# Optimization experiments

Hardware: AMD Instinct MI355X
Metric: run time of the kernel (lower is better)

The kernel has to match this reference:

```python
import jax, jax.numpy as jnp
import numpy as np
import math

# Model dims
B, S, D, H = 2, 2048, 1024, 16
DH = D // H  # 64
TAU = 0.2
EPS = 1e-5

# Unit-scaling scale factors (constraint = gmean of fwd/bwd scales)
# Linear: gmean(fan_in**-0.5, fan_out**-0.5) = (fan_in*fan_out)**-0.25
# Matmul (m,k)@(k,n): gmean(k**-0.5, n**-0.5, m**-0.5) = (m*k*n)**(-1/6)
# Softmax over dim n: gmean(n/1.31, n/1.65) (empirical constants from unit_scaling)
# GELU: gmean(1/0.588, 1/0.675)
MM_SCALE = (S * S * DH) ** (-1.0 / 6.0)
SM_SCALE = S / math.sqrt(1.31 * 1.65)
GELU_SCALE = (0.588 * 0.675) ** -0.5
SQRT_TAU = math.sqrt(TAU)
SQRT_1MTAU = math.sqrt(1.0 - TAU)


def u_linear(x, w, b=None):
    fan_out, fan_in = w.shape
    scale = (fan_in * fan_out) ** -0.25
    y = x @ w.T
    if b is not None:
        y = y + b
    return y * scale


def layer_norm(x, w, b):
    m = jnp.mean(x, axis=-1, keepdims=True)
    v = jnp.mean(jnp.square(x - m), axis=-1, keepdims=True)
    return (x - m) * jax.lax.rsqrt(v + EPS) * w + b


def setup_inputs() -> dict:
    key = jax.random.key(0)
    ks = jax.random.split(key, 8)
    return {
        "x": jax.random.normal(ks[0], (B, S, D), jnp.float32),
        "w_qkv": jax.random.normal(ks[1], (3 * D, D), jnp.float32),
        "w_o": jax.random.normal(ks[2], (D, D), jnp.float32),
        "w1": jax.random.normal(ks[3], (4 * D, D), jnp.float32),
        "b1": jnp.zeros((4 * D,), jnp.float32),
        "w2": jax.random.normal(ks[4], (D, 4 * D), jnp.float32),
        "b2": jnp.zeros((D,), jnp.float32),
        "ln1_w": jnp.ones((D,), jnp.float32),
        "ln1_b": jnp.zeros((D,), jnp.float32),
        "ln2_w": jnp.ones((D,), jnp.float32),
        "ln2_b": jnp.zeros((D,), jnp.float32),
    }


def reference(x, w_qkv, w_o, w1, b1, w2, b2, ln1_w, ln1_b, ln2_w, ln2_b):
    # --- MHSA branch (residual_split forward is identity; tau enters at add) ---
    skip = x
    h = layer_norm(x, ln1_w, ln1_b)
    qkv = u_linear(h, w_qkv)  # [B,S,3D]
    # einops 'b s (d z h) -> z b h s d' with z=3, h=H
    qkv = qkv.reshape(B, S, DH, 3, H)
    q = jnp.transpose(qkv[:, :, :, 0, :], (0, 3, 1, 2))  # [B,H,S,DH]
    k = jnp.transpose(qkv[:, :, :, 1, :], (0, 3, 1, 2))
    v = jnp.transpose(qkv[:, :, :, 2, :], (0, 3, 1, 2))
    scores = jnp.einsum("bhsd,bhtd->bhst", q, k) * MM_SCALE
    attn = jax.nn.softmax(scores, axis=-1) * SM_SCALE
    # dropout: eval mode -> identity
    av = jnp.einsum("bhst,bhtd->bhsd", attn, v) * MM_SCALE
    av = jnp.transpose(av, (0, 2, 1, 3)).reshape(B, S, D)  # b h s d -> b s (h d)
    attn_out = u_linear(av, w_o)
    x = SQRT_TAU * attn_out + SQRT_1MTAU * skip  # residual_add

    # --- MLP branch ---
    skip = x
    h = layer_norm(x, ln2_w, ln2_b)
    h = u_linear(h, w1, b1)
    h = jax.nn.gelu(h, approximate=False) * GELU_SCALE
    h = u_linear(h, w2, b2)
    return SQRT_TAU * h + SQRT_1MTAU * skip
```

## Files before the change

kernel.cpp:

```cpp
#include <hip/hip_runtime.h>
#include <hip/hip_bf16.h>
#include <math.h>

typedef __hip_bfloat16 bf16;
typedef __attribute__((ext_vector_type(8))) short short8;
typedef __attribute__((ext_vector_type(4))) float floatx4;

#define B_   2
#define S_   2048
#define D_   1024
#define H_   16
#define DH_  64
#define BS_  4096
#define D3_  3072
#define DF_  4096

__device__ __forceinline__ float tof(float v) { return v; }
__device__ __forceinline__ float tof(bf16 v) { return __bfloat162float(v); }

__device__ __forceinline__ void gload_lds16(const bf16* g, bf16* l) {
  __builtin_amdgcn_global_load_lds(
      (const __attribute__((address_space(1))) unsigned int*)g,
      (__attribute__((address_space(3))) unsigned int*)l, 16, 0, 0);
}

#define VMCNT(n) asm volatile("s_waitcnt vmcnt(" #n ")" ::: "memory")

__global__ __launch_bounds__(256) void cvt_f32_bf16(
    const float* __restrict__ in, bf16* __restrict__ out, int n4) {
  int i = blockIdx.x * 256 + threadIdx.x;
  if (i >= n4) return;
  float4 v = ((const float4*)in)[i];
  bf16 o[4] = {__float2bfloat16(v.x), __float2bfloat16(v.y),
               __float2bfloat16(v.z), __float2bfloat16(v.w)};
  ((ulong1*)out)[i] = *(ulong1*)o;
}

__global__ __launch_bounds__(256) void cvt_qkv_o(
    const float* __restrict__ wqkv, const float* __restrict__ wo,
    bf16* __restrict__ wqb, bf16* __restrict__ wob) {
  const int g = blockIdx.x * 256 + threadIdx.x;
  if (g < 786432) {
    const int n2 = g >> 8;
    const int col = (g & 255) * 4;
    const int z = n2 >> 10, hh = (n2 >> 6) & 15, d = n2 & 63;
    const int n = d * 48 + z * 16 + hh;
    float4 v = *(const float4*)(wqkv + (size_t)n * 1024 + col);
    bf16 o[4] = {__float2bfloat16(v.x), __float2bfloat16(v.y),
                 __float2bfloat16(v.z), __float2bfloat16(v.w)};
    *(unsigned long long*)(wqb + (size_t)n2 * 1024 + col) =
        *(unsigned long long*)o;
  } else {
    const int g2 = g - 786432;
    float4 v = ((const float4*)wo)[g2];
    bf16 o[4] = {__float2bfloat16(v.x), __float2bfloat16(v.y),
                 __float2bfloat16(v.z), __float2bfloat16(v.w)};
    ((unsigned long long*)wob)[g2] = *(unsigned long long*)o;
  }
}

template <bool FUSE, bool INIT, typename TA, typename TS>
__global__ __launch_bounds__(256) void resid_ln_kernel(
    const TA* __restrict__ a, const TA* __restrict__ a2,
    const TS* __restrict__ skip,
    const float* __restrict__ w, const float* __restrict__ bias,
    bf16* __restrict__ hout, float st, float s1t,
    float* __restrict__ oinit, const float* __restrict__ b2,
    float cb, float cs) {
  const int row = blockIdx.x;
  const int tid = threadIdx.x;
  const int base = tid * 4;
  const size_t roff = (size_t)row * D_;

  float xv[4];
#pragma unroll
  for (int i = 0; i < 4; i++) {
    float v = tof(a[roff + base + i]);
    if (FUSE) v = st * (v + tof(a2[roff + base + i]))
                  + s1t * tof(skip[roff + base + i]);
    xv[i] = v;
  }
  if (INIT) {
#pragma unroll
    for (int i = 0; i < 4; i++)
      oinit[roff + base + i] = cs * xv[i] + cb * b2[base + i];
  }

  float ls = 0.f, lq = 0.f;
#pragma unroll
  for (int i = 0; i < 4; i++) { ls += xv[i]; lq += xv[i] * xv[i]; }

  __shared__ float ssum[256];
  __shared__ float ssq[256];
  ssum[tid] = ls; ssq[tid] = lq;
  __syncthreads();
  for (int off = 128; off > 0; off >>= 1) {
    if (tid < off) { ssum[tid] += ssum[tid + off]; ssq[tid] += ssq[tid + off]; }
    __syncthreads();
  }
  const float mean = ssum[0] * (1.0f / D_);
  const float var  = ssq[0] * (1.0f / D_) - mean * mean;
  const float rstd = rsqrtf(var + 1e-5f);

#pragma unroll
  for (int i = 0; i < 4; i++) {
    float v = (xv[i] - mean) * rstd * w[base + i] + bias[base + i];
    hout[roff + base + i] = __float2bfloat16(v);
  }
}

__global__ __launch_bounds__(256) void reduce_ffn2(
    const bf16* __restrict__ p0, const bf16* __restrict__ p1,
    float* __restrict__ out, float sc) {
  const size_t i = ((size_t)blockIdx.x * 256 + threadIdx.x) * 8;
  short8 a = *(const short8*)(p0 + i);
  short8 b = *(const short8*)(p1 + i);
  bf16 t0[8], t1[8];
  *(short8*)t0 = a; *(short8*)t1 = b;
  float4 o0 = *(float4*)(out + i);
  float4 o1 = *(float4*)(out + i + 4);
#pragma unroll
  for (int e = 0; e < 4; e++) {
    ((float*)&o0)[e] += sc * (__bfloat162float(t0[e]) + __bfloat162float(t1[e]));
    ((float*)&o1)[e] += sc * (__bfloat162float(t0[e + 4]) + __bfloat162float(t1[e + 4]));
  }
  *(float4*)(out + i) = o0;
  *(float4*)(out + i + 4) = o1;
}

template <int EPI, int NSPLIT, typename TC>
__global__ __launch_bounds__(512, 2) void gemm_mfma256(
    const bf16* __restrict__ A, const bf16* __restrict__ Bw,
    TC* __restrict__ C, int M, int N, int K, float scale,
    const float* __restrict__ bias, float st) {
  __shared__ __align__(16) bf16 As[2][2][128][64];
  __shared__ __align__(16) bf16 Bs[2][2][128][64];

  const int tid = threadIdx.x;
  const int lane = tid & 63;
  const int w = tid >> 6;
  const int wm = w >> 2;
  const int wn = w & 3;
  const int quad = lane >> 4;
  const int l16 = lane & 15;

  const int nbx = N >> 8;
  const int nwg = nbx * (M >> 8) * NSPLIT;
  int bid = blockIdx.x;
  bid = (bid & 7) * (nwg >> 3) + (bid >> 3);
  const int split = bid & (NSPLIT - 1);
  const int tile = bid / NSPLIT;
  const size_t bm = (size_t)(tile / nbx) * 256;
  const size_t bn = (size_t)(tile % nbx) * 256;
  const int lda = K * NSPLIT;
  const int koff = split * K;

  const bf16* gsrc[4][2];
  bf16* ldsp[4][2];
#pragma unroll
  for (int i = 0; i < 2; i++) {
    const int G = tid + i * 512;
    const int cr = G >> 3;
    const int gs8 = ((G & 7) ^ (cr & 7)) * 8;
    const int ra = ((cr >> 6) << 7) + (cr & 63);
    const int rb = ((cr >> 5) << 6) + (cr & 31);
    gsrc[0][i] = A  + (bm + ra) * (size_t)lda + koff + gs8;
    gsrc[2][i] = A  + (bm + ra + 64) * (size_t)lda + koff + gs8;
    gsrc[1][i] = Bw + (bn + rb) * (size_t)lda + koff + gs8;
    gsrc[3][i] = Bw + (bn + rb + 32) * (size_t)lda + koff + gs8;
    ldsp[0][i] = &As[0][0][0][0] + G * 8;
    ldsp[2][i] = &As[0][1][0][0] + G * 8;
    ldsp[1][i] = &Bs[0][0][0][0] + G * 8;
    ldsp[3][i] = &Bs[0][1][0][0] + G * 8;
  }

  auto STAGE = [&](int c, int tn) {
    const int boff = (tn & 1) * 16384;
    gload_lds16(gsrc[c][0] + (size_t)tn * 64, ldsp[c][0] + boff);
    gload_lds16(gsrc[c][1] + (size_t)tn * 64, ldsp[c][1] + boff);
  };

  const int ksw0 = (quad ^ (l16 & 7)) * 8;
  const int ksw1 = ((4 + quad) ^ (l16 & 7)) * 8;

  floatx4 acc[8][4];
#pragma unroll
  for (int i = 0; i < 8; i++)
#pragma unroll
    for (int j = 0; j < 4; j++) acc[i][j] = {0.f, 0.f, 0.f, 0.f};

  short8 af[4][2], bv[2][2];

  auto READ_A = [&](int b, int h) {
#pragma unroll
    for (int mf = 0; mf < 4; mf++) {
      const bf16* p = &As[b][h][wm * 64 + mf * 16 + l16][0];
      af[mf][0] = *(const short8*)(p + ksw0);
      af[mf][1] = *(const short8*)(p + ksw1);
    }
  };
  auto READ_B = [&](int b, int bh) {
#pragma unroll
    for (int nf = 0; nf < 2; nf++) {
      const bf16* p = &Bs[b][bh][wn * 32 + nf * 16 + l16][0];
      bv[nf][0] = *(const short8*)(p + ksw0);
      bv[nf][1] = *(const short8*)(p + ksw1);
    }
  };
  auto MFMA16 = [&](int mb, int nb) {
#pragma unroll
    for (int mf = 0; mf < 4; mf++)
#pragma unroll
      for (int nf = 0; nf < 2; nf++) {
        floatx4 c = acc[mb + mf][nb + nf];
        c = __builtin_amdgcn_mfma_f32_16x16x32_bf16(af[mf][0], bv[nf][0], c, 0, 0, 0);
        c = __builtin_amdgcn_mfma_f32_16x16x32_bf16(af[mf][1], bv[nf][1], c, 0, 0, 0);
        acc[mb + mf][nb + nf] = c;
      }
  };

  STAGE(0, 0); STAGE(1, 0); STAGE(2, 0); STAGE(3, 0);
  VMCNT(4);
  __builtin_amdgcn_s_barrier();
  __builtin_amdgcn_sched_barrier(0);

  const int NT = K >> 6;
#pragma unroll 1
  for (int t = 0; t < NT; t++) {
    const int b = t & 1;
    const bool nl = (t + 1 < NT);
    READ_A(b, 0);
    READ_B(b, 0);
    if (nl) STAGE(0, t + 1);
    __builtin_amdgcn_s_barrier();
    __builtin_amdgcn_sched_barrier(0);
    __builtin_amdgcn_s_setprio(1);
    MFMA16(0, 0);
    __builtin_amdgcn_s_setprio(0);
    if (nl) { VMCNT(2); } else { VMCNT(0); }
    __builtin_amdgcn_s_barrier();
    __builtin_amdgcn_sched_barrier(0);
    READ_B(b, 1);
    if (nl) STAGE(1, t + 1);
    __builtin_amdgcn_s_barrier();
    __builtin_amdgcn_sched_barrier(0);
    __builtin_amdgcn_s_setprio(1);
    MFMA16(0, 2);
    __builtin_amdgcn_s_setprio(0);
    __builtin_amdgcn_s_barrier();
    __builtin_amdgcn_sched_barrier(0);
    READ_A(b, 1);
    if (nl) STAGE(2, t + 1);
    __builtin_amdgcn_s_barrier();
    __builtin_amdgcn_sched_barrier(0);
    __builtin_amdgcn_s_setprio(1);
    MFMA16(4, 2);
    __builtin_amdgcn_s_setprio(0);
    __builtin_amdgcn_s_barrier();
    __builtin_amdgcn_sched_barrier(0);
    READ_B(b, 0);
    if (nl) STAGE(3, t + 1);
    __builtin_amdgcn_s_barrier();
    __builtin_amdgcn_sched_barrier(0);
    __builtin_amdgcn_s_setprio(1);
    MFMA16(4, 0);
    __builtin_amdgcn_s_setprio(0);
    if (nl) { VMCNT(4); } else { VMCNT(0); }
    __builtin_amdgcn_s_barrier();
    __builtin_amdgcn_sched_barrier(0);
  }

  float sc_eff = scale;
  if (EPI == 2) sc_eff = (bn < 1024) ? st : scale;
  float bias4[4];
  if (EPI == 1) {
#pragma unroll
    for (int j = 0; j < 4; j++) bias4[j] = bias[bn + wn * 64 + j * 16 + l16];
  }
  const size_t poff = (size_t)split * M * N;
#pragma unroll
  for (int mi = 0; mi < 8; mi++) {
    const size_t r0 = bm + wm * 128 + (mi >> 2) * 64 + (mi & 3) * 16 + quad * 4;
#pragma unroll
    for (int r = 0; r < 4; r++) {
      const size_t rowoff = (r0 + r) * (size_t)N + bn + wn * 64 + l16;
#pragma unroll
      for (int j = 0; j < 4; j++) {
        float v = acc[mi][j][r];
        if (EPI == 0 || EPI == 2) {
          ((bf16*)C)[rowoff + j * 16] = __float2bfloat16(v * sc_eff);
        } else if (EPI == 1) {
          float u = (v + bias4[j]) * scale;
          float tt = u * (0.7978845608f + 0.0356774081f * u * u);
          float e = __builtin_amdgcn_exp2f(tt * 2.8853900818f);
          float th = 1.0f - 2.0f * __builtin_amdgcn_rcpf(e + 1.0f);
          ((bf16*)C)[rowoff + j * 16] =
              __float2bfloat16(0.5f * u * (1.0f + th) * st);
        } else if (EPI == 3) {
          ((float*)C)[poff + rowoff + j * 16] = v * scale;
        } else {
          ((bf16*)C)[poff + rowoff + j * 16] = __float2bfloat16(v);
        }
      }
    }
  }
}

__global__ __launch_bounds__(512) void flash_attn_mfma(
    const bf16* __restrict__ qkv, bf16* __restrict__ att, float out_scale) {
  const int qb = blockIdx.x * 128;
  const int h = blockIdx.y, b = blockIdx.z;
  const int tid = threadIdx.x;
  const int lane = tid & 63;
  const int wv = tid >> 6;
  const int quad = lane >> 4;
  const int l16 = lane & 15;

  __shared__ __align__(16) bf16 Ks[2][64][72];
  __shared__ __align__(16) bf16 Vt[2][64][72];
  __shared__ __align__(16) bf16 Ps[128][64];

  const bf16* Qb_ = qkv + (size_t)b * S_ * D3_ + h * DH_;
  const bf16* Kb_ = Qb_ + 1024;
  const bf16* Vb_ = Qb_ + 2048;

  short8 bq0, bq1;
  {
    const bf16* qrow = Qb_ + (size_t)(qb + wv * 16 + l16) * D3_ + quad * 8;
    bq0 = *(const short8*)(qrow);
    bq1 = *(const short8*)(qrow + 32);
  }

  float l_part = 0.f;
  floatx4 o[4];
#pragma unroll
  for (int fd = 0; fd < 4; fd++) o[fd] = {0.f, 0.f, 0.f, 0.f};

  const int prow = wv * 16 + l16;
  const int psw = (prow & 7) << 4;
  char* pbase = (char*)&Ps[0][0] + prow * 128;

  const int kr = tid >> 3, ko = (tid & 7) * 8;
  const int vj = tid & 63, vd = (tid >> 6) * 8;

  uint4 kreg = *(const uint4*)(Kb_ + (size_t)kr * D3_ + ko);
  uint4 vreg = *(const uint4*)(Vb_ + (size_t)vj * D3_ + vd);

  int cur = 0;
  for (int t = 0; t < S_ / 64; t++) {
    *(uint4*)&Ks[cur][kr][ko] = kreg;
    {
      bf16 tmp[8];
      *(uint4*)tmp = vreg;
#pragma unroll
      for (int e = 0; e < 8; e++) Vt[cur][vd + e][vj] = tmp[e];
    }
    __syncthreads();

    {
      const int tn = (t + 1 < S_ / 64) ? t + 1 : t;
      kreg = *(const uint4*)(Kb_ + (size_t)(tn * 64 + kr) * D3_ + ko);
      vreg = *(const uint4*)(Vb_ + (size_t)(tn * 64 + vj) * D3_ + vd);
    }

    float st[4][4];
    __builtin_amdgcn_s_setprio(1);
#pragma unroll
    for (int fk = 0; fk < 4; fk++) {
      short8 ak0 = *(const short8*)&Ks[cur][fk * 16 + l16][quad * 8];
      short8 ak1 = *(const short8*)&Ks[cur][fk * 16 + l16][32 + quad * 8];
      floatx4 acc = {0.f, 0.f, 0.f, 0.f};
      acc = __builtin_amdgcn_mfma_f32_16x16x32_bf16(ak0, bq0, acc, 0, 0, 0);
      acc = __builtin_amdgcn_mfma_f32_16x16x32_bf16(ak1, bq1, acc, 0, 0, 0);
#pragma unroll
      for (int r = 0; r < 4; r++) st[fk][r] = acc[r];
    }
    __builtin_amdgcn_s_setprio(0);

#pragma unroll
    for (int fk = 0; fk < 4; fk++) {
      bf16 pk[4];
#pragma unroll
      for (int r = 0; r < 4; r++) {
        const float p = exp2f(st[fk][r]);
        l_part += p;
        pk[r] = __float2bfloat16(p);
      }
      *(uint2*)(pbase + ((fk * 32 + quad * 8) ^ psw)) = *(uint2*)pk;
    }

    short8 ap0 = *(const short8*)(pbase + ((quad * 16) ^ psw));
    short8 ap1 = *(const short8*)(pbase + ((64 + quad * 16) ^ psw));
    __builtin_amdgcn_s_setprio(1);
#pragma unroll
    for (int fd = 0; fd < 4; fd++) {
      short8 bv0 = *(const short8*)&Vt[cur][fd * 16 + l16][quad * 8];
      short8 bv1 = *(const short8*)&Vt[cur][fd * 16 + l16][32 + quad * 8];
      o[fd] = __builtin_amdgcn_mfma_f32_16x16x32_bf16(ap0, bv0, o[fd], 0, 0, 0);
      o[fd] = __builtin_amdgcn_mfma_f32_16x16x32_bf16(ap1, bv1, o[fd], 0, 0, 0);
    }
    __builtin_amdgcn_s_setprio(0);

    cur ^= 1;
  }

  l_part += __shfl_xor(l_part, 16);
  l_part += __shfl_xor(l_part, 32);
#pragma unroll
  for (int r = 0; r < 4; r++) {
    const float lq = __shfl(l_part, quad * 4 + r, 64);
    const float sc = out_scale / lq;
    const size_t base =
        ((size_t)(b * S_ + qb + wv * 16 + quad * 4 + r)) * D_ + h * DH_;
#pragma unroll
    for (int fd = 0; fd < 4; fd++)
      att[base + fd * 16 + l16] = __float2bfloat16(o[fd][r] * sc);
  }
}

extern "C" void kernel_launch(void* const* d_in, const int* in_sizes, int n_in,
                              void* d_out, int out_size, void* d_ws, size_t ws_size,
                              hipStream_t stream) {
  const float* x     = (const float*)d_in[0];
  const float* w_qkv = (const float*)d_in[1];
  const float* w_o   = (const float*)d_in[2];
  const float* w1    = (const float*)d_in[3];
  const float* b1    = (const float*)d_in[4];
  const float* w2    = (const float*)d_in[5];
  const float* b2    = (const float*)d_in[6];
  const float* ln1w  = (const float*)d_in[7];
  const float* ln1b  = (const float*)d_in[8];
  const float* ln2w  = (const float*)d_in[9];
  const float* ln2b  = (const float*)d_in[10];
  float* out = (float*)d_out;
  bf16* ws  = (bf16*)d_ws;

  bf16* h1   = ws;
  bf16* wqb  = ws + 4194304;
  bf16* qkv  = ws + 8388608;
  bf16* att  = ws + 20971520;
  bf16* wob  = ws + 25165824;
  float* Po  = (float*)ws;
  bf16* w1b  = ws + 16777216;
  bf16* h2   = ws + 20971520;
  bf16* g    = ws;
  bf16* w2b  = ws + 16777216;
  bf16* Pf   = ws + 20971520;

  const float MM_SCALE   = (float)pow((double)S_ * S_ * DH_, -1.0 / 6.0);
  const float SM_SCALE   = (float)((double)S_ / sqrt(1.31 * 1.65));
  const float GELU_SCALE = (float)pow(0.588 * 0.675, -0.5);
  const float SQRT_TAU   = (float)sqrt(0.2);
  const float SQRT_1MT   = (float)sqrt(0.8);
  const float LOG2E      = 1.4426950408889634f;
  const float qkv_scale  = (float)pow((double)D_ * D3_, -0.25);
  const float o_scale    = (float)pow((double)D_ * D_, -0.25);
  const float w1_scale   = (float)pow((double)D_ * DF_, -0.25);
  const float w2_scale   = (float)pow((double)DF_ * D_, -0.25);

  cvt_qkv_o<<<4096, 256, 0, stream>>>(w_qkv, w_o, wqb, wob);
  resid_ln_kernel<false, false, float, float><<<BS_, 256, 0, stream>>>(
      x, nullptr, nullptr, ln1w, ln1b, h1, 0.f, 0.f, nullptr, nullptr, 0.f, 0.f);
  gemm_mfma256<2, 1, bf16><<<dim3(192), 512, 0, stream>>>(
      h1, wqb, qkv, BS_, D3_, D_, qkv_scale, nullptr,
      qkv_scale * MM_SCALE * LOG2E);
  flash_attn_mfma<<<dim3(S_ / 128, H_, B_), 512, 0, stream>>>(
      qkv, att, SM_SCALE * MM_SCALE);
  cvt_f32_bf16<<<(DF_ * D_ / 4 + 255) / 256, 256, 0, stream>>>(w1, w1b, DF_ * D_ / 4);
  gemm_mfma256<3, 2, float><<<dim3(128), 512, 0, stream>>>(
      att, wob, Po, BS_, D_, D_ / 2, o_scale, nullptr, 0.f);
  resid_ln_kernel<true, true, float, float><<<BS_, 256, 0, stream>>>(
      Po, Po + (size_t)BS_ * D_, x, ln2w, ln2b, h2, SQRT_TAU, SQRT_1MT,
      out, b2, SQRT_TAU * w2_scale, SQRT_1MT);
  gemm_mfma256<1, 1, bf16><<<dim3(256), 512, 0, stream>>>(
      h2, w1b, g, BS_, DF_, D_, w1_scale, b1, GELU_SCALE);
  cvt_f32_bf16<<<(D_ * DF_ / 4 + 255) / 256, 256, 0, stream>>>(w2, w2b, D_ * DF_ / 4);
  gemm_mfma256<4, 2, bf16><<<dim3(128), 512, 0, stream>>>(
      g, w2b, Pf, BS_, D_, DF_ / 2, 1.f, nullptr, 0.f);
  reduce_ffn2<<<2048, 256, 0, stream>>>(
      Pf, Pf + (size_t)BS_ * D_, out, SQRT_TAU * w2_scale);
}
```

Measured before the change: 371.5 us.

## Add 256x128 split-K GEMM for N=1024 projections and rework flash attention loads

Adds a gemm_mfma128 kernel with 256x128 tiles and two blocks per CU, used for the attention-output and FFN2 split-K GEMMs so 256 workgroups run instead of 128. Flash attention now loads K through direct global-to-LDS copies with an XOR swizzle. It computes the softmax row sum with an extra MFMA against a ones column appended to V, replacing the per-thread adds and shuffles. Blocks are remapped so neighbouring workgroups share heads, and exp2 uses the hardware builtin. The costs are one extra MFMA per step, a larger V buffer in LDS, and more register pressure in the new GEMM.

```diff
diff --git a/kernel.cpp b/kernel.cpp
--- a/kernel.cpp
+++ b/kernel.cpp
@@ -277,7 +277,6 @@
 #pragma unroll
     for (int j = 0; j < 4; j++) bias4[j] = bias[bn + wn * 64 + j * 16 + l16];
   }
-  const size_t poff = (size_t)split * M * N;
 #pragma unroll
   for (int mi = 0; mi < 8; mi++) {
     const size_t r0 = bm + wm * 128 + (mi >> 2) * 64 + (mi & 3) * 16 + quad * 4;
@@ -287,16 +286,176 @@
 #pragma unroll
       for (int j = 0; j < 4; j++) {
         float v = acc[mi][j][r];
-        if (EPI == 0 || EPI == 2) {
+        if (EPI == 2 || EPI == 0) {
           ((bf16*)C)[rowoff + j * 16] = __float2bfloat16(v * sc_eff);
-        } else if (EPI == 1) {
+        } else {
           float u = (v + bias4[j]) * scale;
           float tt = u * (0.7978845608f + 0.0356774081f * u * u);
           float e = __builtin_amdgcn_exp2f(tt * 2.8853900818f);
           float th = 1.0f - 2.0f * __builtin_amdgcn_rcpf(e + 1.0f);
           ((bf16*)C)[rowoff + j * 16] =
               __float2bfloat16(0.5f * u * (1.0f + th) * st);
-        } else if (EPI == 3) {
+        }
+      }
+    }
+  }
+}
+
+template <int EPI, typename TC>
+__global__ __launch_bounds__(512, 2) void gemm_mfma128(
+    const bf16* __restrict__ A, const bf16* __restrict__ Bw,
+    TC* __restrict__ C, int M, int N, int K, float scale) {
+  __shared__ __align__(16) bf16 As[2][2][128][64];
+  __shared__ __align__(16) bf16 Bs[2][2][64][64];
+
+  const int tid = threadIdx.x;
+  const int lane = tid & 63;
+  const int w = tid >> 6;
+  const int wm = w >> 2;
+  const int wn = w & 3;
+  const int quad = lane >> 4;
+  const int l16 = lane & 15;
+
+  const int nbx = N >> 7;
+  const int nwg = nbx * (M >> 8) * 2;
+  int bid = blockIdx.x;
+  bid = (bid & 7) * (nwg >> 3) + (bid >> 3);
+  const int split = bid & 1;
+  const int tile = bid >> 1;
+  const size_t bm = (size_t)(tile / nbx) * 256;
+  const size_t bn = (size_t)(tile % nbx) * 128;
+  const int lda = K * 2;
+  const int koff = split * K;
+
+  const bf16* gA[2][2];
+  bf16* lA[2][2];
+#pragma unroll
+  for (int i = 0; i < 2; i++) {
+    const int G = tid + i * 512;
+    const int cr = G >> 3;
+    const int gs8 = ((G & 7) ^ (cr & 7)) * 8;
+    const int ra = ((cr >> 6) << 7) + (cr & 63);
+    gA[0][i] = A + (bm + ra) * (size_t)lda + koff + gs8;
+    gA[1][i] = A + (bm + ra + 64) * (size_t)lda + koff + gs8;
+    lA[0][i] = &As[0][0][0][0] + G * 8;
+    lA[1][i] = &As[0][1][0][0] + G * 8;
+  }
+  const bf16* gB[2];
+  bf16* lB[2];
+  {
+    const int cr = tid >> 3;
+    const int gs8 = ((tid & 7) ^ (cr & 7)) * 8;
+    gB[0] = Bw + (bn + cr) * (size_t)lda + koff + gs8;
+    gB[1] = Bw + (bn + 64 + cr) * (size_t)lda + koff + gs8;
+    lB[0] = &Bs[0][0][0][0] + tid * 8;
+    lB[1] = &Bs[0][1][0][0] + tid * 8;
+  }
+
+  auto STAGE_A = [&](int h, int tn) {
+    const int boff = (tn & 1) * 16384;
+    gload_lds16(gA[h][0] + (size_t)tn * 64, lA[h][0] + boff);
+    gload_lds16(gA[h][1] + (size_t)tn * 64, lA[h][1] + boff);
+  };
+  auto STAGE_B = [&](int bh, int tn) {
+    const int boff = (tn & 1) * 8192;
+    gload_lds16(gB[bh] + (size_t)tn * 64, lB[bh] + boff);
+  };
+
+  const int ksw0 = (quad ^ (l16 & 7)) * 8;
+  const int ksw1 = ((4 + quad) ^ (l16 & 7)) * 8;
+
+  floatx4 acc[8][2];
+#pragma unroll
+  for (int i = 0; i < 8; i++)
+#pragma unroll
+    for (int j = 0; j < 2; j++) acc[i][j] = {0.f, 0.f, 0.f, 0.f};
+
+  short8 af[4][2], bv[2][2];
+
+  auto READ_A = [&](int b, int h) {
+#pragma unroll
+    for (int mf = 0; mf < 4; mf++) {
+      const bf16* p = &As[b][h][wm * 64 + mf * 16 + l16][0];
+      af[mf][0] = *(const short8*)(p + ksw0);
+      af[mf][1] = *(const short8*)(p + ksw1);
+    }
+  };
+  auto READ_BNF = [&](int b, int nf) {
+    const bf16* p = &Bs[b][wn >> 1][(wn & 1) * 32 + nf * 16 + l16][0];
+    bv[nf][0] = *(const short8*)(p + ksw0);
+    bv[nf][1] = *(const short8*)(p + ksw1);
+  };
+  auto MFMA8 = [&](int mb, int nf) {
+#pragma unroll
+    for (int mf = 0; mf < 4; mf++) {
+      floatx4 c = acc[mb + mf][nf];
+      c = __builtin_amdgcn_mfma_f32_16x16x32_bf16(af[mf][0], bv[nf][0], c, 0, 0, 0);
+      c = __builtin_amdgcn_mfma_f32_16x16x32_bf16(af[mf][1], bv[nf][1], c, 0, 0, 0);
+      acc[mb + mf][nf] = c;
+    }
+  };
+
+  STAGE_A(0, 0); STAGE_B(0, 0); STAGE_B(1, 0); STAGE_A(1, 0);
+  VMCNT(2);
+  __builtin_amdgcn_s_barrier();
+  __builtin_amdgcn_sched_barrier(0);
+
+  const int NT = K >> 6;
+#pragma unroll 1
+  for (int t = 0; t < NT; t++) {
+    const int b = t & 1;
+    const bool nl = (t + 1 < NT);
+    READ_A(b, 0);
+    READ_BNF(b, 0);
+    if (nl) STAGE_A(0, t + 1);
+    __builtin_amdgcn_s_barrier();
+    __builtin_amdgcn_sched_barrier(0);
+    __builtin_amdgcn_s_setprio(1);
+    MFMA8(0, 0);
+    __builtin_amdgcn_s_setprio(0);
+    __builtin_amdgcn_s_barrier();
+    __builtin_amdgcn_sched_barrier(0);
+    READ_BNF(b, 1);
+    if (nl) STAGE_B(0, t + 1);
+    __builtin_amdgcn_s_barrier();
+    __builtin_amdgcn_sched_barrier(0);
+    __builtin_amdgcn_s_setprio(1);
+    MFMA8(0, 1);
+    __builtin_amdgcn_s_setprio(0);
+    if (nl) { VMCNT(3); } else { VMCNT(0); }
+    __builtin_amdgcn_s_barrier();
+    __builtin_amdgcn_sched_barrier(0);
+    READ_A(b, 1);
+    if (nl) STAGE_B(1, t + 1);
+    __builtin_amdgcn_s_barrier();
+    __builtin_amdgcn_sched_barrier(0);
+    __builtin_amdgcn_s_setprio(1);
+    MFMA8(4, 1);
+    __builtin_amdgcn_s_setprio(0);
+    __builtin_amdgcn_s_barrier();
+    __builtin_amdgcn_sched_barrier(0);
+    if (nl) STAGE_A(1, t + 1);
+    __builtin_amdgcn_s_barrier();
+    __builtin_amdgcn_sched_barrier(0);
+    __builtin_amdgcn_s_setprio(1);
+    MFMA8(4, 0);
+    __builtin_amdgcn_s_setprio(0);
+    if (nl) { VMCNT(2); } else { VMCNT(0); }
+    __builtin_amdgcn_s_barrier();
+    __builtin_amdgcn_sched_barrier(0);
+  }
+
+  const size_t poff = (size_t)split * M * N;
+#pragma unroll
+  for (int mi = 0; mi < 8; mi++) {
+    const size_t r0 = bm + wm * 128 + (mi >> 2) * 64 + (mi & 3) * 16 + quad * 4;
+#pragma unroll
+    for (int r = 0; r < 4; r++) {
+      const size_t rowoff = (r0 + r) * (size_t)N + bn + wn * 32 + l16;
+#pragma unroll
+      for (int j = 0; j < 2; j++) {
+        float v = acc[mi][j][r];
+        if (EPI == 3) {
           ((float*)C)[poff + rowoff + j * 16] = v * scale;
         } else {
           ((bf16*)C)[poff + rowoff + j * 16] = __float2bfloat16(v);
@@ -308,21 +467,30 @@
 
 __global__ __launch_bounds__(512) void flash_attn_mfma(
     const bf16* __restrict__ qkv, bf16* __restrict__ att, float out_scale) {
-  const int qb = blockIdx.x * 128;
-  const int h = blockIdx.y, b = blockIdx.z;
+  const int flat = (blockIdx.z * H_ + blockIdx.y) * (S_ / 128) + blockIdx.x;
+  const int g8 = flat & 7, slot = flat >> 3;
+  const int hf = g8 * 4 + (slot >> 4);
+  const int qb = (slot & 15) * 128;
+  const int h = hf & 15, b = hf >> 4;
+
   const int tid = threadIdx.x;
   const int lane = tid & 63;
   const int wv = tid >> 6;
   const int quad = lane >> 4;
   const int l16 = lane & 15;
 
-  __shared__ __align__(16) bf16 Ks[2][64][72];
-  __shared__ __align__(16) bf16 Vt[2][64][72];
+  __shared__ __align__(16) bf16 Ks[2][64][64];
+  __shared__ __align__(16) bf16 Vt[2][80][72];
   __shared__ __align__(16) bf16 Ps[128][64];
 
   const bf16* Qb_ = qkv + (size_t)b * S_ * D3_ + h * DH_;
   const bf16* Kb_ = Qb_ + 1024;
   const bf16* Vb_ = Qb_ + 2048;
+
+  for (int i = tid; i < 2 * 16 * 72; i += 512) {
+    const int bb = i / (16 * 72), rr = (i / 72) % 16, cc = i % 72;
+    Vt[bb][64 + rr][cc] = __float2bfloat16(rr == 0 ? 1.f : 0.f);
+  }
 
   short8 bq0, bq1;
   {
@@ -331,24 +499,27 @@
     bq1 = *(const short8*)(qrow + 32);
   }
 
-  float l_part = 0.f;
-  floatx4 o[4];
-#pragma unroll
-  for (int fd = 0; fd < 4; fd++) o[fd] = {0.f, 0.f, 0.f, 0.f};
+  floatx4 o[5];
+#pragma unroll
+  for (int fd = 0; fd < 5; fd++) o[fd] = {0.f, 0.f, 0.f, 0.f};
 
   const int prow = wv * 16 + l16;
   const int psw = (prow & 7) << 4;
   char* pbase = (char*)&Ps[0][0] + prow * 128;
 
-  const int kr = tid >> 3, ko = (tid & 7) * 8;
+  const bf16* ksrc =
+      Kb_ + (size_t)(tid >> 3) * D3_ + (((tid & 7) ^ ((tid >> 3) & 7)) * 8);
+  bf16* kdst = &Ks[0][0][0] + tid * 8;
   const int vj = tid & 63, vd = (tid >> 6) * 8;
 
-  uint4 kreg = *(const uint4*)(Kb_ + (size_t)kr * D3_ + ko);
+  const int ksw0 = (quad ^ (l16 & 7)) * 8;
+  const int ksw1 = ((4 + quad) ^ (l16 & 7)) * 8;
+
+  gload_lds16(ksrc, kdst);
   uint4 vreg = *(const uint4*)(Vb_ + (size_t)vj * D3_ + vd);
 
   int cur = 0;
   for (int t = 0; t < S_ / 64; t++) {
-    *(uint4*)&Ks[cur][kr][ko] = kreg;
     {
       bf16 tmp[8];
       *(uint4*)tmp = vreg;
@@ -357,18 +528,18 @@
     }
     __syncthreads();
 
-    {
-      const int tn = (t + 1 < S_ / 64) ? t + 1 : t;
-      kreg = *(const uint4*)(Kb_ + (size_t)(tn * 64 + kr) * D3_ + ko);
-      vreg = *(const uint4*)(Vb_ + (size_t)(tn * 64 + vj) * D3_ + vd);
+    if (t + 1 < S_ / 64) {
+      gload_lds16(ksrc + (size_t)(t + 1) * 64 * D3_, kdst + (cur ^ 1) * 4096);
+      vreg = *(const uint4*)(Vb_ + (size_t)((t + 1) * 64 + vj) * D3_ + vd);
     }
 
     float st[4][4];
     __builtin_amdgcn_s_setprio(1);
 #pragma unroll
     for (int fk = 0; fk < 4; fk++) {
-      short8 ak0 = *(const short8*)&Ks[cur][fk * 16 + l16][quad * 8];
-      short8 ak1 = *(const short8*)&Ks[cur][fk * 16 + l16][32 + quad * 8];
+      const bf16* kp = &Ks[cur][fk * 16 + l16][0];
+      short8 ak0 = *(const short8*)(kp + ksw0);
+      short8 ak1 = *(const short8*)(kp + ksw1);
       floatx4 acc = {0.f, 0.f, 0.f, 0.f};
       acc = __builtin_amdgcn_mfma_f32_16x16x32_bf16(ak0, bq0, acc, 0, 0, 0);
       acc = __builtin_amdgcn_mfma_f32_16x16x32_bf16(ak1, bq1, acc, 0, 0, 0);
@@ -381,11 +552,8 @@
     for (int fk = 0; fk < 4; fk++) {
       bf16 pk[4];
 #pragma unroll
-      for (int r = 0; r < 4; r++) {
-        const float p = exp2f(st[fk][r]);
-        l_part += p;
-        pk[r] = __float2bfloat16(p);
-      }
+      for (int r = 0; r < 4; r++)
+        pk[r] = __float2bfloat16(__builtin_amdgcn_exp2f(st[fk][r]));
       *(uint2*)(pbase + ((fk * 32 + quad * 8) ^ psw)) = *(uint2*)pk;
     }
 
@@ -393,7 +561,7 @@
     short8 ap1 = *(const short8*)(pbase + ((64 + quad * 16) ^ psw));
     __builtin_amdgcn_s_setprio(1);
 #pragma unroll
-    for (int fd = 0; fd < 4; fd++) {
+    for (int fd = 0; fd < 5; fd++) {
       short8 bv0 = *(const short8*)&Vt[cur][fd * 16 + l16][quad * 8];
       short8 bv1 = *(const short8*)&Vt[cur][fd * 16 + l16][32 + quad * 8];
       o[fd] = __builtin_amdgcn_mfma_f32_16x16x32_bf16(ap0, bv0, o[fd], 0, 0, 0);
@@ -404,11 +572,9 @@
     cur ^= 1;
   }
 
-  l_part += __shfl_xor(l_part, 16);
-  l_part += __shfl_xor(l_part, 32);
 #pragma unroll
   for (int r = 0; r < 4; r++) {
-    const float lq = __shfl(l_part, quad * 4 + r, 64);
+    const float lq = __shfl(o[4][r], quad << 4, 64);
     const float sc = out_scale / lq;
     const size_t base =
         ((size_t)(b * S_ + qb + wv * 16 + quad * 4 + r)) * D_ + h * DH_;
@@ -467,16 +633,16 @@
   flash_attn_mfma<<<dim3(S_ / 128, H_, B_), 512, 0, stream>>>(
       qkv, att, SM_SCALE * MM_SCALE);
   cvt_f32_bf16<<<(DF_ * D_ / 4 + 255) / 256, 256, 0, stream>>>(w1, w1b, DF_ * D_ / 4);
-  gemm_mfma256<3, 2, float><<<dim3(128), 512, 0, stream>>>(
-      att, wob, Po, BS_, D_, D_ / 2, o_scale, nullptr, 0.f);
+  gemm_mfma128<3, float><<<dim3(256), 512, 0, stream>>>(
+      att, wob, Po, BS_, D_, D_ / 2, o_scale);
   resid_ln_kernel<true, true, float, float><<<BS_, 256, 0, stream>>>(
       Po, Po + (size_t)BS_ * D_, x, ln2w, ln2b, h2, SQRT_TAU, SQRT_1MT,
       out, b2, SQRT_TAU * w2_scale, SQRT_1MT);
   gemm_mfma256<1, 1, bf16><<<dim3(256), 512, 0, stream>>>(
       h2, w1b, g, BS_, DF_, D_, w1_scale, b1, GELU_SCALE);
   cvt_f32_bf16<<<(D_ * DF_ / 4 + 255) / 256, 256, 0, stream>>>(w2, w2b, D_ * DF_ / 4);
-  gemm_mfma256<4, 2, bf16><<<dim3(128), 512, 0, stream>>>(
-      g, w2b, Pf, BS_, D_, DF_ / 2, 1.f, nullptr, 0.f);
+  gemm_mfma128<4, bf16><<<dim3(256), 512, 0, stream>>>(
+      g, w2b, Pf, BS_, D_, DF_ / 2, 1.f);
   reduce_ffn2<<<2048, 256, 0, stream>>>(
       Pf, Pf + (size_t)BS_ * D_, out, SQRT_TAU * w2_scale);
 }
```

New measurement: 348.4 us. 1.07x faster.
